# Kernel optimization log

Hardware: AMD Instinct MI355X
Metric: run time of the kernel (lower is better)

The kernel has to match this reference:

```python
import jax, jax.numpy as jnp
import numpy as np

B, N, C, K, D, H = 4, 16000, 128, 16, 4, 512
EPS = 1e-5


def _bn(x, g, b, m, v):
    # eval-mode BatchNorm1d over channel dim (applied to flattened B*N rows)
    return (x - m) * jax.lax.rsqrt(v + EPS) * g + b


def _ffn(x, W1, b1, W2, g, b, m, v):
    h = jax.nn.gelu(jnp.einsum('bnc,ch->bnh', x, W1) + b1)
    y = jnp.einsum('bnh,hc->bnc', h, W2)  # second linear has no bias
    return _bn(y, g, b, m, v)


def _vector_feature(x, knn):
    # knn edge max-pooling: max_k ( x[b, knn[b,n,k], :] - x[b, n, :] )
    gathered = jnp.take_along_axis(x[:, :, None, :], knn[:, :, :, None], axis=1)  # (B,N,K,C)
    return jnp.max(gathered - x[:, :, None, :], axis=2)


def _vfr(x, knn, W, g, b, m, v):
    y = jnp.einsum('bnc,cd->bnd', x, W)
    y = _vector_feature(y, knn)
    return _bn(y, g, b, m, v)


def setup_inputs():
    key = jax.random.key(0)
    ks = jax.random.split(key, 16)
    s = 0.05
    return {
        'x': jax.random.normal(ks[0], (B, N, C), jnp.float32),
        'pe': jax.random.normal(ks[1], (B, N, C), jnp.float32),
        'knn': jax.random.randint(ks[2], (B, N, K), 0, N, dtype=jnp.int32),
        # mlp (the single leading FFN)
        'mlp_W1': jax.random.normal(ks[3], (C, H), jnp.float32) * s,
        'mlp_b1': jnp.zeros((H,), jnp.float32),
        'mlp_W2': jax.random.normal(ks[4], (H, C), jnp.float32) * s,
        'mlp_g': jax.random.uniform(ks[5], (C,), jnp.float32, 0.5, 1.5),
        'mlp_beta': jnp.zeros((C,), jnp.float32),
        'mlp_m': jnp.zeros((C,), jnp.float32),
        'mlp_v': jnp.ones((C,), jnp.float32),
        # per-depth VFR params (stacked over depth D)
        'vfr_W': jax.random.normal(ks[6], (D, C, C), jnp.float32) * s,
        'vfr_g': jax.random.uniform(ks[7], (D, C), jnp.float32, 0.5, 1.5),
        'vfr_beta': jnp.zeros((D, C), jnp.float32),
        'vfr_m': jnp.zeros((D, C), jnp.float32),
        'vfr_v': jnp.ones((D, C), jnp.float32),
        # per-depth FFN params
        'ffn_W1': jax.random.normal(ks[8], (D, C, H), jnp.float32) * s,
        'ffn_b1': jnp.zeros((D, H), jnp.float32),
        'ffn_W2': jax.random.normal(ks[9], (D, H, C), jnp.float32) * s,
        'ffn_g': jax.random.uniform(ks[10], (D, C), jnp.float32, 0.5, 1.5),
        'ffn_beta': jnp.zeros((D, C), jnp.float32),
        'ffn_m': jnp.zeros((D, C), jnp.float32),
        'ffn_v': jnp.ones((D, C), jnp.float32),
    }


def reference(x, pe, knn,
              mlp_W1, mlp_b1, mlp_W2, mlp_g, mlp_beta, mlp_m, mlp_v,
              vfr_W, vfr_g, vfr_beta, vfr_m, vfr_v,
              ffn_W1, ffn_b1, ffn_W2, ffn_g, ffn_beta, ffn_m, ffn_v):
    # drop_path is identity in eval mode
    x = x + _ffn(x, mlp_W1, mlp_b1, mlp_W2, mlp_g, mlp_beta, mlp_m, mlp_v)
    for i in range(D):
        x = x + pe
        x = x + _vfr(x, knn, vfr_W[i], vfr_g[i], vfr_beta[i], vfr_m[i], vfr_v[i])
        x = x + _ffn(x, ffn_W1[i], ffn_b1[i], ffn_W2[i], ffn_g[i], ffn_beta[i], ffn_m[i], ffn_v[i])
    return x
```

## Files before the change

kernel.cpp:

```cpp
#include <hip/hip_runtime.h>
#include <hip/hip_bf16.h>

typedef __attribute__((ext_vector_type(8))) short bf16x8;
typedef __attribute__((ext_vector_type(4))) short bf16x4;
typedef __attribute__((ext_vector_type(4))) float f32x4;

#define B_ 4
#define N_ 16000
#define C_ 128
#define K_ 16
#define D_ 4
#define H_ 512
#define R_ (B_*N_)
#define EPSV 1e-5f

__device__ __forceinline__ ushort f2bf(float f) {
    uint32_t b = __builtin_bit_cast(uint32_t, f);
    b += 0x7fffu + ((b >> 16) & 1u);
    return (ushort)(b >> 16);
}
__device__ __forceinline__ float bf2f(ushort u) {
    return __builtin_bit_cast(float, (uint32_t)u << 16);
}
__device__ __forceinline__ float gelu_fast(float v) {
    float v2 = v * v;
    float u = v * fmaf(0.0356774081f, v2, 0.7978845608f);
    float e = __expf(-2.0f * u);
    return v * __builtin_amdgcn_rcpf(1.0f + e);
}
__device__ __forceinline__ void gll16(const void* g, void* l) {
    __builtin_amdgcn_global_load_lds(
        (__attribute__((address_space(1))) void*)g,
        (__attribute__((address_space(3))) void*)l, 16, 0, 0);
}

__global__ void prep_kernel(
    const float* __restrict__ mlp_W1, const float* __restrict__ mlp_b1,
    const float* __restrict__ mlp_W2, const float* __restrict__ mlp_g,
    const float* __restrict__ mlp_be, const float* __restrict__ mlp_m,
    const float* __restrict__ mlp_v,
    const float* __restrict__ vfr_W, const float* __restrict__ vfr_g,
    const float* __restrict__ vfr_be, const float* __restrict__ vfr_m,
    const float* __restrict__ vfr_v,
    const float* __restrict__ ffn_W1, const float* __restrict__ ffn_b1,
    const float* __restrict__ ffn_W2, const float* __restrict__ ffn_g,
    const float* __restrict__ ffn_be, const float* __restrict__ ffn_m,
    const float* __restrict__ ffn_v,
    ushort* __restrict__ w1t, ushort* __restrict__ w2p, ushort* __restrict__ wvs,
    float* __restrict__ b1a, float* __restrict__ fs, float* __restrict__ fb,
    float* __restrict__ vs, float* __restrict__ vb)
{
    int i = blockIdx.x * 256 + threadIdx.x;
    const int NW = 5 * H_ * C_;
    if (i < NW) {
        int f = i / (H_*C_), e = i % (H_*C_);
        int h = e / C_, c = e % C_;
        const float* src = (f == 0) ? mlp_W1 : ffn_W1 + (size_t)(f-1)*C_*H_;
        w1t[i] = f2bf(src[(size_t)c*H_ + h]);
        return;
    }
    i -= NW;
    if (i < NW) {
        int f = i / (H_*C_), e = i % (H_*C_);
        int c = e / H_, p = e % H_;
        int s = p & 31, lam = s >> 3, j = s & 7;
        int h = (p & ~31) + lam*4 + (j & 3) + ((j >> 2) << 4);
        const float* src = (f == 0) ? mlp_W2 : ffn_W2 + (size_t)(f-1)*H_*C_;
        w2p[i] = f2bf(src[(size_t)h*C_ + c]);
        return;
    }
    i -= NW;
    if (i < D_*C_*C_) {
        int d = i / (C_*C_), e = i % (C_*C_);
        int co = e / C_, p = e % C_;
        int s = p & 31, lam = s >> 3, j = s & 7;
        int k = (p & ~31) + lam*4 + (j & 3) + ((j >> 2) << 4);
        wvs[i] = f2bf(vfr_W[(size_t)d*C_*C_ + (size_t)k*C_ + co]);
        return;
    }
    i -= D_*C_*C_;
    if (i < 5*H_) {
        int f = i / H_, h = i % H_;
        b1a[i] = (f == 0) ? mlp_b1[h] : ffn_b1[(f-1)*H_ + h];
        return;
    }
    i -= 5*H_;
    if (i < 5*C_) {
        int f = i / C_, c = i % C_;
        float g  = (f==0) ? mlp_g[c]  : ffn_g[(f-1)*C_ + c];
        float be = (f==0) ? mlp_be[c] : ffn_be[(f-1)*C_ + c];
        float m  = (f==0) ? mlp_m[c]  : ffn_m[(f-1)*C_ + c];
        float v  = (f==0) ? mlp_v[c]  : ffn_v[(f-1)*C_ + c];
        float s = g * rsqrtf(v + EPSV);
        fs[i] = s; fb[i] = be - m * s;
        return;
    }
    i -= 5*C_;
    if (i < D_*C_) {
        float s = vfr_g[i] * rsqrtf(vfr_v[i] + EPSV);
        vs[i] = s; vb[i] = vfr_be[i] - vfr_m[i] * s;
    }
}

template<bool ADD_PE, bool NEXT_T>
__global__ __launch_bounds__(256, 4) void ffn_kernel(
    const float* __restrict__ xin, float* __restrict__ xout,
    const float* __restrict__ pe,
    const ushort* __restrict__ W1t,
    const ushort* __restrict__ W2p,
    const float* __restrict__ b1,
    const float* __restrict__ bns, const float* __restrict__ bnb,
    const ushort* __restrict__ Wvs,
    ushort* __restrict__ tout)
{
    __shared__ __attribute__((aligned(16))) char lds[32768];
    char* W1s = lds;
    char* W2s = lds + 16384;

    const int tid  = threadIdx.x;
    const int m0   = blockIdx.x * 64;
    const int wv   = tid >> 6;
    const int lane = tid & 63;
    const int lr   = lane & 15;
    const int lh   = lane >> 4;

    bf16x8 xa[4];
    {
        const float* xrow = xin + (size_t)(m0 + wv*16 + lr) * C_ + lh*8;
        #pragma unroll
        for (int kk = 0; kk < 4; ++kk) {
            float4 v0 = *(const float4*)(xrow + kk*32);
            float4 v1 = *(const float4*)(xrow + kk*32 + 4);
            bf16x8 pk;
            pk[0]=(short)f2bf(v0.x); pk[1]=(short)f2bf(v0.y);
            pk[2]=(short)f2bf(v0.z); pk[3]=(short)f2bf(v0.w);
            pk[4]=(short)f2bf(v1.x); pk[5]=(short)f2bf(v1.y);
            pk[6]=(short)f2bf(v1.z); pk[7]=(short)f2bf(v1.w);
            xa[kk] = pk;
        }
    }

    f32x4 acc2[8];
    #pragma unroll
    for (int i = 0; i < 8; ++i) acc2[i] = (f32x4){0.f,0.f,0.f,0.f};

    for (int hc = 0; hc < 8; ++hc) {
        const int h0 = hc * 64;
        __syncthreads();
        #pragma unroll
        for (int i = 0; i < 4; ++i) {
            int row = i*16 + wv*4 + (lane >> 4);
            const char* src = (const char*)(W1t + (size_t)(h0 + row) * C_)
                            + (((lane & 15) * 16) ^ ((row & 7) << 4));
            gll16(src, W1s + i*4096 + wv*1024);
        }
        #pragma unroll
        for (int i = 0; i < 4; ++i) {
            int row = i*32 + wv*8 + (lane >> 3);
            const char* src = (const char*)(W2p + (size_t)row * H_ + h0)
                            + (((lane & 7) * 16) ^ ((row & 7) << 4));
            gll16(src, W2s + i*4096 + wv*1024);
        }
        __syncthreads();

        f32x4 acc1[4];
        #pragma unroll
        for (int i = 0; i < 4; ++i) acc1[i] = (f32x4){0.f,0.f,0.f,0.f};
        #pragma unroll
        for (int kk = 0; kk < 4; ++kk) {
            int kb = kk*64 + lh*16;
            #pragma unroll
            for (int nf = 0; nf < 4; ++nf) {
                int rb = nf*16 + lr;
                bf16x8 w1 = *(bf16x8*)(W1s + rb*256 + (kb ^ ((rb&7)<<4)));
                acc1[nf] = __builtin_amdgcn_mfma_f32_16x16x32_bf16(w1, xa[kk], acc1[nf], 0, 0, 0);
            }
        }
        bf16x4 pa[4];
        #pragma unroll
        for (int nf = 0; nf < 4; ++nf) {
            float4 bias = *(const float4*)(b1 + h0 + nf*16 + lh*4);
            bf16x4 p;
            p[0] = (short)f2bf(gelu_fast(acc1[nf][0] + bias.x));
            p[1] = (short)f2bf(gelu_fast(acc1[nf][1] + bias.y));
            p[2] = (short)f2bf(gelu_fast(acc1[nf][2] + bias.z));
            p[3] = (short)f2bf(gelu_fast(acc1[nf][3] + bias.w));
            pa[nf] = p;
        }
        #pragma unroll
        for (int g = 0; g < 2; ++g) {
            bf16x8 af = __builtin_shufflevector(pa[2*g], pa[2*g+1], 0,1,2,3,4,5,6,7);
            int kb = g*64 + lh*16;
            #pragma unroll
            for (int nf = 0; nf < 8; ++nf) {
                int rb = nf*16 + lr;
                bf16x8 w2 = *(bf16x8*)(W2s + rb*128 + (kb ^ ((rb&7)<<4)));
                acc2[nf] = __builtin_amdgcn_mfma_f32_16x16x32_bf16(w2, af, acc2[nf], 0, 0, 0);
            }
        }
    }

    if (NEXT_T) {
        __syncthreads();
        #pragma unroll
        for (int i = 0; i < 8; ++i) {
            int r = i*16 + wv*4 + (lane >> 4);
            const char* src = (const char*)(Wvs + (size_t)r * C_)
                            + (((lane & 15) * 16) ^ ((r & 7) << 4));
            gll16(src, lds + i*4096 + wv*1024);
        }
    }

    const int row = m0 + wv*16 + lr;
    bf16x4 pa2[8];
    #pragma unroll
    for (int nf = 0; nf < 8; ++nf) {
        int c0 = nf*16 + lh*4;
        float4 sv = *(const float4*)(bns + c0);
        float4 bv = *(const float4*)(bnb + c0);
        float4 xi = *(const float4*)(xin + (size_t)row * C_ + c0);
        if (ADD_PE) {
            float4 pv = *(const float4*)(pe + (size_t)row * C_ + c0);
            xi.x += pv.x; xi.y += pv.y; xi.z += pv.z; xi.w += pv.w;
        }
        float4 xo;
        xo.x = xi.x + acc2[nf][0] * sv.x + bv.x;
        xo.y = xi.y + acc2[nf][1] * sv.y + bv.y;
        xo.z = xi.z + acc2[nf][2] * sv.z + bv.z;
        xo.w = xi.w + acc2[nf][3] * sv.w + bv.w;
        *(float4*)(xout + (size_t)row * C_ + c0) = xo;
        if (NEXT_T) {
            bf16x4 p;
            p[0] = (short)f2bf(xo.x); p[1] = (short)f2bf(xo.y);
            p[2] = (short)f2bf(xo.z); p[3] = (short)f2bf(xo.w);
            pa2[nf] = p;
        }
    }

    if (NEXT_T) {
        __syncthreads();
        f32x4 acc3[8];
        #pragma unroll
        for (int i = 0; i < 8; ++i) acc3[i] = (f32x4){0.f,0.f,0.f,0.f};
        #pragma unroll
        for (int g = 0; g < 4; ++g) {
            bf16x8 af = __builtin_shufflevector(pa2[2*g], pa2[2*g+1], 0,1,2,3,4,5,6,7);
            int kb = g*64 + lh*16;
            #pragma unroll
            for (int nf = 0; nf < 8; ++nf) {
                int rb = nf*16 + lr;
                bf16x8 b = *(bf16x8*)(lds + rb*256 + (kb ^ ((rb&7)<<4)));
                acc3[nf] = __builtin_amdgcn_mfma_f32_16x16x32_bf16(af, b, acc3[nf], 0, 0, 0);
            }
        }
        #pragma unroll
        for (int nf = 0; nf < 8; ++nf) {
            int col = nf*16 + lr;
            #pragma unroll
            for (int j = 0; j < 4; ++j) {
                int trow = m0 + wv*16 + lh*4 + j;
                tout[(size_t)trow * C_ + col] = f2bf(acc3[nf][j]);
            }
        }
    }
}

__global__ __launch_bounds__(256) void vfr_gather_kernel(
    float* __restrict__ x, const ushort* __restrict__ t,
    const int* __restrict__ knn,
    const float* __restrict__ s, const float* __restrict__ bb)
{
    const int wv   = threadIdx.x >> 6;
    const int lane = threadIdx.x & 63;
    const int p = blockIdx.x * 4 + wv;
    const int b = p / N_;
    const int base = b * N_;
    const int* kp = knn + (size_t)p * K_;
    const uint* trow = (const uint*)t;

    uint cen = trow[(size_t)p * 64 + lane];
    float c0 = bf2f((ushort)(cen & 0xffffu));
    float c1 = bf2f((ushort)(cen >> 16));
    float m0v = -INFINITY, m1v = -INFINITY;
    #pragma unroll
    for (int k = 0; k < K_; ++k) {
        int idx = kp[k];
        uint g = trow[(size_t)(base + idx) * 64 + lane];
        m0v = fmaxf(m0v, bf2f((ushort)(g & 0xffffu)));
        m1v = fmaxf(m1v, bf2f((ushort)(g >> 16)));
    }
    m0v -= c0; m1v -= c1;

    int c = lane * 2;
    float2 sv = *(const float2*)(s + c);
    float2 bv = *(const float2*)(bb + c);
    size_t o = (size_t)p * C_ + c;
    float2 xv = *(const float2*)(x + o);
    xv.x += m0v * sv.x + bv.x;
    xv.y += m1v * sv.y + bv.y;
    *(float2*)(x + o) = xv;
}

extern "C" void kernel_launch(void* const* d_in, const int* in_sizes, int n_in,
                              void* d_out, int out_size, void* d_ws, size_t ws_size,
                              hipStream_t stream) {
    const float* x      = (const float*)d_in[0];
    const float* pe     = (const float*)d_in[1];
    const int*   knn    = (const int*)d_in[2];
    const float* mlp_W1 = (const float*)d_in[3];
    const float* mlp_b1 = (const float*)d_in[4];
    const float* mlp_W2 = (const float*)d_in[5];
    const float* mlp_g  = (const float*)d_in[6];
    const float* mlp_be = (const float*)d_in[7];
    const float* mlp_m  = (const float*)d_in[8];
    const float* mlp_v  = (const float*)d_in[9];
    const float* vfr_W  = (const float*)d_in[10];
    const float* vfr_g  = (const float*)d_in[11];
    const float* vfr_be = (const float*)d_in[12];
    const float* vfr_m  = (const float*)d_in[13];
    const float* vfr_v  = (const float*)d_in[14];
    const float* ffn_W1 = (const float*)d_in[15];
    const float* ffn_b1 = (const float*)d_in[16];
    const float* ffn_W2 = (const float*)d_in[17];
    const float* ffn_g  = (const float*)d_in[18];
    const float* ffn_be = (const float*)d_in[19];
    const float* ffn_m  = (const float*)d_in[20];
    const float* ffn_v  = (const float*)d_in[21];
    float* out = (float*)d_out;

    char* ws = (char*)d_ws;
    ushort* tbuf = (ushort*)ws;  ws += (size_t)R_ * C_ * 2;
    ushort* w1t  = (ushort*)ws;  ws += (size_t)5 * H_ * C_ * 2;
    ushort* w2p  = (ushort*)ws;  ws += (size_t)5 * C_ * H_ * 2;
    ushort* wvs  = (ushort*)ws;  ws += (size_t)D_ * C_ * C_ * 2;
    float*  b1a  = (float*)ws;   ws += (size_t)5 * H_ * 4;
    float*  fs   = (float*)ws;   ws += (size_t)5 * C_ * 4;
    float*  fb   = (float*)ws;   ws += (size_t)5 * C_ * 4;
    float*  vs   = (float*)ws;   ws += (size_t)D_ * C_ * 4;
    float*  vb   = (float*)ws;   ws += (size_t)D_ * C_ * 4;

    const int prep_items = 2*(5*H_*C_) + D_*C_*C_ + 5*H_ + 5*C_ + D_*C_;
    prep_kernel<<<(prep_items + 255) / 256, 256, 0, stream>>>(
        mlp_W1, mlp_b1, mlp_W2, mlp_g, mlp_be, mlp_m, mlp_v,
        vfr_W, vfr_g, vfr_be, vfr_m, vfr_v,
        ffn_W1, ffn_b1, ffn_W2, ffn_g, ffn_be, ffn_m, ffn_v,
        w1t, w2p, wvs, b1a, fs, fb, vs, vb);

    ffn_kernel<true, true><<<R_/64, 256, 0, stream>>>(
        x, out, pe, w1t, w2p, b1a, fs, fb, wvs, tbuf);

    for (int d = 0; d < D_; ++d) {
        vfr_gather_kernel<<<R_/4, 256, 0, stream>>>(
            out, tbuf, knn, vs + d * C_, vb + d * C_);
        if (d < D_ - 1) {
            ffn_kernel<true, true><<<R_/64, 256, 0, stream>>>(
                out, out, pe,
                w1t + (size_t)(d+1) * H_ * C_, w2p + (size_t)(d+1) * C_ * H_,
                b1a + (d+1) * H_, fs + (d+1) * C_, fb + (d+1) * C_,
                wvs + (size_t)(d+1) * C_ * C_, tbuf);
        } else {
            ffn_kernel<false, false><<<R_/64, 256, 0, stream>>>(
                out, out, pe,
                w1t + (size_t)(d+1) * H_ * C_, w2p + (size_t)(d+1) * C_ * H_,
                b1a + (d+1) * H_, fs + (d+1) * C_, fb + (d+1) * C_,
                wvs, tbuf);
        }
    }
}
```

Baseline: 350.9 us.

## Double the FFN row tile and double-buffer weight chunks in LDS

Each FFN block now handles 128 rows instead of 64, with each wave computing two 16-row M tiles. Every weight fragment read from LDS therefore feeds two MFMAs, halving weight staging traffic per row. The weight chunks are double-buffered in a 64KB LDS region so the next chunk's global-to-LDS load overlaps the current chunk's compute, leaving one barrier per iteration. In exchange register pressure roughly doubles, launch bounds drop to 2 blocks per CU, and the grid halves to 500 blocks, which may reduce occupancy and latency hiding.

```diff
diff --git a/kernel.cpp b/kernel.cpp
--- a/kernel.cpp
+++ b/kernel.cpp
@@ -21,6 +21,9 @@
 }
 __device__ __forceinline__ float bf2f(ushort u) {
     return __builtin_bit_cast(float, (uint32_t)u << 16);
+}
+__device__ __forceinline__ uint pk2bf(float lo, float hi) {
+    return (uint)f2bf(lo) | ((uint)f2bf(hi) << 16);
 }
 __device__ __forceinline__ float gelu_fast(float v) {
     float v2 = v * v;
@@ -103,7 +106,7 @@
 }
 
 template<bool ADD_PE, bool NEXT_T>
-__global__ __launch_bounds__(256, 4) void ffn_kernel(
+__global__ __launch_bounds__(256, 2) void ffn_kernel(
     const float* __restrict__ xin, float* __restrict__ xout,
     const float* __restrict__ pe,
     const ushort* __restrict__ W1t,
@@ -113,59 +116,72 @@
     const ushort* __restrict__ Wvs,
     ushort* __restrict__ tout)
 {
-    __shared__ __attribute__((aligned(16))) char lds[32768];
-    char* W1s = lds;
-    char* W2s = lds + 16384;
+    __shared__ __attribute__((aligned(16))) char lds[65536];
 
     const int tid  = threadIdx.x;
-    const int m0   = blockIdx.x * 64;
+    const int m0   = blockIdx.x * 128;
     const int wv   = tid >> 6;
     const int lane = tid & 63;
     const int lr   = lane & 15;
     const int lh   = lane >> 4;
 
-    bf16x8 xa[4];
-    {
-        const float* xrow = xin + (size_t)(m0 + wv*16 + lr) * C_ + lh*8;
-        #pragma unroll
-        for (int kk = 0; kk < 4; ++kk) {
-            float4 v0 = *(const float4*)(xrow + kk*32);
-            float4 v1 = *(const float4*)(xrow + kk*32 + 4);
-            bf16x8 pk;
-            pk[0]=(short)f2bf(v0.x); pk[1]=(short)f2bf(v0.y);
-            pk[2]=(short)f2bf(v0.z); pk[3]=(short)f2bf(v0.w);
-            pk[4]=(short)f2bf(v1.x); pk[5]=(short)f2bf(v1.y);
-            pk[6]=(short)f2bf(v1.z); pk[7]=(short)f2bf(v1.w);
-            xa[kk] = pk;
-        }
-    }
-
-    f32x4 acc2[8];
-    #pragma unroll
-    for (int i = 0; i < 8; ++i) acc2[i] = (f32x4){0.f,0.f,0.f,0.f};
-
-    for (int hc = 0; hc < 8; ++hc) {
+    auto stageW = [&](int hc, int buf) {
+        char* base = lds + buf * 32768;
         const int h0 = hc * 64;
-        __syncthreads();
         #pragma unroll
         for (int i = 0; i < 4; ++i) {
             int row = i*16 + wv*4 + (lane >> 4);
             const char* src = (const char*)(W1t + (size_t)(h0 + row) * C_)
                             + (((lane & 15) * 16) ^ ((row & 7) << 4));
-            gll16(src, W1s + i*4096 + wv*1024);
+            gll16(src, base + i*4096 + wv*1024);
         }
         #pragma unroll
         for (int i = 0; i < 4; ++i) {
             int row = i*32 + wv*8 + (lane >> 3);
             const char* src = (const char*)(W2p + (size_t)row * H_ + h0)
                             + (((lane & 7) * 16) ^ ((row & 7) << 4));
-            gll16(src, W2s + i*4096 + wv*1024);
-        }
-        __syncthreads();
-
-        f32x4 acc1[4];
-        #pragma unroll
-        for (int i = 0; i < 4; ++i) acc1[i] = (f32x4){0.f,0.f,0.f,0.f};
+            gll16(src, base + 16384 + i*4096 + wv*1024);
+        }
+    };
+
+    stageW(0, 0);
+
+    bf16x8 xa[2][4];
+    #pragma unroll
+    for (int mt = 0; mt < 2; ++mt) {
+        const float* xrow = xin + (size_t)(m0 + wv*32 + mt*16 + lr) * C_ + lh*8;
+        #pragma unroll
+        for (int kk = 0; kk < 4; ++kk) {
+            float4 v0 = *(const float4*)(xrow + kk*32);
+            float4 v1 = *(const float4*)(xrow + kk*32 + 4);
+            uint p0 = pk2bf(v0.x, v0.y), p1 = pk2bf(v0.z, v0.w);
+            uint p2 = pk2bf(v1.x, v1.y), p3 = pk2bf(v1.z, v1.w);
+            uint4 u = {p0, p1, p2, p3};
+            xa[mt][kk] = __builtin_bit_cast(bf16x8, u);
+        }
+    }
+
+    f32x4 acc2[2][8];
+    #pragma unroll
+    for (int mt = 0; mt < 2; ++mt)
+        #pragma unroll
+        for (int i = 0; i < 8; ++i) acc2[mt][i] = (f32x4){0.f,0.f,0.f,0.f};
+
+    __syncthreads();
+
+    for (int hc = 0; hc < 8; ++hc) {
+        const int h0  = hc * 64;
+        const int buf = hc & 1;
+        if (hc < 7) stageW(hc + 1, buf ^ 1);
+
+        char* W1s = lds + buf * 32768;
+        char* W2s = W1s + 16384;
+
+        f32x4 acc1[2][4];
+        #pragma unroll
+        for (int mt = 0; mt < 2; ++mt)
+            #pragma unroll
+            for (int i = 0; i < 4; ++i) acc1[mt][i] = (f32x4){0.f,0.f,0.f,0.f};
         #pragma unroll
         for (int kk = 0; kk < 4; ++kk) {
             int kb = kk*64 + lh*16;
@@ -173,35 +189,48 @@
             for (int nf = 0; nf < 4; ++nf) {
                 int rb = nf*16 + lr;
                 bf16x8 w1 = *(bf16x8*)(W1s + rb*256 + (kb ^ ((rb&7)<<4)));
-                acc1[nf] = __builtin_amdgcn_mfma_f32_16x16x32_bf16(w1, xa[kk], acc1[nf], 0, 0, 0);
-            }
-        }
-        bf16x4 pa[4];
+                #pragma unroll
+                for (int mt = 0; mt < 2; ++mt)
+                    acc1[mt][nf] = __builtin_amdgcn_mfma_f32_16x16x32_bf16(
+                        w1, xa[mt][kk], acc1[mt][nf], 0, 0, 0);
+            }
+        }
+        bf16x4 pa[2][4];
         #pragma unroll
         for (int nf = 0; nf < 4; ++nf) {
             float4 bias = *(const float4*)(b1 + h0 + nf*16 + lh*4);
-            bf16x4 p;
-            p[0] = (short)f2bf(gelu_fast(acc1[nf][0] + bias.x));
-            p[1] = (short)f2bf(gelu_fast(acc1[nf][1] + bias.y));
-            p[2] = (short)f2bf(gelu_fast(acc1[nf][2] + bias.z));
-            p[3] = (short)f2bf(gelu_fast(acc1[nf][3] + bias.w));
-            pa[nf] = p;
+            #pragma unroll
+            for (int mt = 0; mt < 2; ++mt) {
+                uint q0 = pk2bf(gelu_fast(acc1[mt][nf][0] + bias.x),
+                                gelu_fast(acc1[mt][nf][1] + bias.y));
+                uint q1 = pk2bf(gelu_fast(acc1[mt][nf][2] + bias.z),
+                                gelu_fast(acc1[mt][nf][3] + bias.w));
+                uint2 u = {q0, q1};
+                pa[mt][nf] = __builtin_bit_cast(bf16x4, u);
+            }
         }
         #pragma unroll
         for (int g = 0; g < 2; ++g) {
-            bf16x8 af = __builtin_shufflevector(pa[2*g], pa[2*g+1], 0,1,2,3,4,5,6,7);
+            bf16x8 af[2];
+            #pragma unroll
+            for (int mt = 0; mt < 2; ++mt)
+                af[mt] = __builtin_shufflevector(pa[mt][2*g], pa[mt][2*g+1],
+                                                 0,1,2,3,4,5,6,7);
             int kb = g*64 + lh*16;
             #pragma unroll
             for (int nf = 0; nf < 8; ++nf) {
                 int rb = nf*16 + lr;
                 bf16x8 w2 = *(bf16x8*)(W2s + rb*128 + (kb ^ ((rb&7)<<4)));
-                acc2[nf] = __builtin_amdgcn_mfma_f32_16x16x32_bf16(w2, af, acc2[nf], 0, 0, 0);
-            }
-        }
+                #pragma unroll
+                for (int mt = 0; mt < 2; ++mt)
+                    acc2[mt][nf] = __builtin_amdgcn_mfma_f32_16x16x32_bf16(
+                        w2, af[mt], acc2[mt][nf], 0, 0, 0);
+            }
+        }
+        __syncthreads();
     }
 
     if (NEXT_T) {
-        __syncthreads();
         #pragma unroll
         for (int i = 0; i < 8; ++i) {
             int r = i*16 + wv*4 + (lane >> 4);
@@ -211,55 +240,68 @@
         }
     }
 
-    const int row = m0 + wv*16 + lr;
-    bf16x4 pa2[8];
+    bf16x4 pa2[2][8];
     #pragma unroll
-    for (int nf = 0; nf < 8; ++nf) {
-        int c0 = nf*16 + lh*4;
-        float4 sv = *(const float4*)(bns + c0);
-        float4 bv = *(const float4*)(bnb + c0);
-        float4 xi = *(const float4*)(xin + (size_t)row * C_ + c0);
-        if (ADD_PE) {
-            float4 pv = *(const float4*)(pe + (size_t)row * C_ + c0);
-            xi.x += pv.x; xi.y += pv.y; xi.z += pv.z; xi.w += pv.w;
-        }
-        float4 xo;
-        xo.x = xi.x + acc2[nf][0] * sv.x + bv.x;
-        xo.y = xi.y + acc2[nf][1] * sv.y + bv.y;
-        xo.z = xi.z + acc2[nf][2] * sv.z + bv.z;
-        xo.w = xi.w + acc2[nf][3] * sv.w + bv.w;
-        *(float4*)(xout + (size_t)row * C_ + c0) = xo;
-        if (NEXT_T) {
-            bf16x4 p;
-            p[0] = (short)f2bf(xo.x); p[1] = (short)f2bf(xo.y);
-            p[2] = (short)f2bf(xo.z); p[3] = (short)f2bf(xo.w);
-            pa2[nf] = p;
+    for (int mt = 0; mt < 2; ++mt) {
+        const int row = m0 + wv*32 + mt*16 + lr;
+        #pragma unroll
+        for (int nf = 0; nf < 8; ++nf) {
+            int c0 = nf*16 + lh*4;
+            float4 sv = *(const float4*)(bns + c0);
+            float4 bv = *(const float4*)(bnb + c0);
+            float4 xi = *(const float4*)(xin + (size_t)row * C_ + c0);
+            if (ADD_PE) {
+                float4 pv = *(const float4*)(pe + (size_t)row * C_ + c0);
+                xi.x += pv.x; xi.y += pv.y; xi.z += pv.z; xi.w += pv.w;
+            }
+            float4 xo;
+            xo.x = xi.x + acc2[mt][nf][0] * sv.x + bv.x;
+            xo.y = xi.y + acc2[mt][nf][1] * sv.y + bv.y;
+            xo.z = xi.z + acc2[mt][nf][2] * sv.z + bv.z;
+            xo.w = xi.w + acc2[mt][nf][3] * sv.w + bv.w;
+            *(float4*)(xout + (size_t)row * C_ + c0) = xo;
+            if (NEXT_T) {
+                uint2 u = {pk2bf(xo.x, xo.y), pk2bf(xo.z, xo.w)};
+                pa2[mt][nf] = __builtin_bit_cast(bf16x4, u);
+            }
         }
     }
 
     if (NEXT_T) {
         __syncthreads();
-        f32x4 acc3[8];
-        #pragma unroll
-        for (int i = 0; i < 8; ++i) acc3[i] = (f32x4){0.f,0.f,0.f,0.f};
+        f32x4 acc3[2][8];
+        #pragma unroll
+        for (int mt = 0; mt < 2; ++mt)
+            #pragma unroll
+            for (int i = 0; i < 8; ++i) acc3[mt][i] = (f32x4){0.f,0.f,0.f,0.f};
         #pragma unroll
         for (int g = 0; g < 4; ++g) {
-            bf16x8 af = __builtin_shufflevector(pa2[2*g], pa2[2*g+1], 0,1,2,3,4,5,6,7);
+            bf16x8 af[2];
+            #pragma unroll
+            for (int mt = 0; mt < 2; ++mt)
+                af[mt] = __builtin_shufflevector(pa2[mt][2*g], pa2[mt][2*g+1],
+                                                 0,1,2,3,4,5,6,7);
             int kb = g*64 + lh*16;
             #pragma unroll
             for (int nf = 0; nf < 8; ++nf) {
                 int rb = nf*16 + lr;
-                bf16x8 b = *(bf16x8*)(lds + rb*256 + (kb ^ ((rb&7)<<4)));
-                acc3[nf] = __builtin_amdgcn_mfma_f32_16x16x32_bf16(af, b, acc3[nf], 0, 0, 0);
-            }
-        }
-        #pragma unroll
-        for (int nf = 0; nf < 8; ++nf) {
-            int col = nf*16 + lr;
-            #pragma unroll
-            for (int j = 0; j < 4; ++j) {
-                int trow = m0 + wv*16 + lh*4 + j;
-                tout[(size_t)trow * C_ + col] = f2bf(acc3[nf][j]);
+                bf16x8 wvf = *(bf16x8*)(lds + rb*256 + (kb ^ ((rb&7)<<4)));
+                #pragma unroll
+                for (int mt = 0; mt < 2; ++mt)
+                    acc3[mt][nf] = __builtin_amdgcn_mfma_f32_16x16x32_bf16(
+                        af[mt], wvf, acc3[mt][nf], 0, 0, 0);
+            }
+        }
+        #pragma unroll
+        for (int mt = 0; mt < 2; ++mt) {
+            #pragma unroll
+            for (int nf = 0; nf < 8; ++nf) {
+                int col = nf*16 + lr;
+                #pragma unroll
+                for (int j = 0; j < 4; ++j) {
+                    int trow = m0 + wv*32 + mt*16 + lh*4 + j;
+                    tout[(size_t)trow * C_ + col] = f2bf(acc3[mt][nf][j]);
+                }
             }
         }
     }
@@ -346,20 +388,20 @@
         ffn_W1, ffn_b1, ffn_W2, ffn_g, ffn_be, ffn_m, ffn_v,
         w1t, w2p, wvs, b1a, fs, fb, vs, vb);
 
-    ffn_kernel<true, true><<<R_/64, 256, 0, stream>>>(
+    ffn_kernel<true, true><<<R_/128, 256, 0, stream>>>(
         x, out, pe, w1t, w2p, b1a, fs, fb, wvs, tbuf);
 
     for (int d = 0; d < D_; ++d) {
         vfr_gather_kernel<<<R_/4, 256, 0, stream>>>(
             out, tbuf, knn, vs + d * C_, vb + d * C_);
         if (d < D_ - 1) {
-            ffn_kernel<true, true><<<R_/64, 256, 0, stream>>>(
+            ffn_kernel<true, true><<<R_/128, 256, 0, stream>>>(
                 out, out, pe,
                 w1t + (size_t)(d+1) * H_ * C_, w2p + (size_t)(d+1) * C_ * H_,
                 b1a + (d+1) * H_, fs + (d+1) * C_, fb + (d+1) * C_,
                 wvs + (size_t)(d+1) * C_ * C_, tbuf);
         } else {
-            ffn_kernel<false, false><<<R_/64, 256, 0, stream>>>(
+            ffn_kernel<false, false><<<R_/128, 256, 0, stream>>>(
                 out, out, pe,
                 w1t + (size_t)(d+1) * H_ * C_, w2p + (size_t)(d+1) * C_ * H_,
                 b1a + (d+1) * H_, fs + (d+1) * C_, fb + (d+1) * C_,
```

Measured after the change: 355.4 us. About the same (+1.3%).

## Read FFN weight fragments directly from global memory instead of staging through LDS

Applied to the files above, without the earlier changes.

Removes the LDS staging of W1, W2 and the VFR weight tiles, along with all block-level barriers in the FFN kernel. Each wave now loads its MFMA weight fragments straight from global memory and relies on L1/L2 caching, since the weights are small and shared by all blocks. This drops the shared memory allocation, which may allow more blocks per CU, and removes barrier stalls. The cost is that four waves each fetch the same weights with less coalesced 16-byte loads. bf16 packing is also rewritten to convert pairs of values into 32-bit words.

```diff
diff --git a/kernel.cpp b/kernel.cpp
--- a/kernel.cpp
+++ b/kernel.cpp
@@ -22,16 +22,14 @@
 __device__ __forceinline__ float bf2f(ushort u) {
     return __builtin_bit_cast(float, (uint32_t)u << 16);
 }
+__device__ __forceinline__ uint pk2bf(float lo, float hi) {
+    return (uint)f2bf(lo) | ((uint)f2bf(hi) << 16);
+}
 __device__ __forceinline__ float gelu_fast(float v) {
     float v2 = v * v;
     float u = v * fmaf(0.0356774081f, v2, 0.7978845608f);
     float e = __expf(-2.0f * u);
     return v * __builtin_amdgcn_rcpf(1.0f + e);
-}
-__device__ __forceinline__ void gll16(const void* g, void* l) {
-    __builtin_amdgcn_global_load_lds(
-        (__attribute__((address_space(1))) void*)g,
-        (__attribute__((address_space(3))) void*)l, 16, 0, 0);
 }
 
 __global__ void prep_kernel(
@@ -113,10 +111,6 @@
     const ushort* __restrict__ Wvs,
     ushort* __restrict__ tout)
 {
-    __shared__ __attribute__((aligned(16))) char lds[32768];
-    char* W1s = lds;
-    char* W2s = lds + 16384;
-
     const int tid  = threadIdx.x;
     const int m0   = blockIdx.x * 64;
     const int wv   = tid >> 6;
@@ -131,14 +125,16 @@
         for (int kk = 0; kk < 4; ++kk) {
             float4 v0 = *(const float4*)(xrow + kk*32);
             float4 v1 = *(const float4*)(xrow + kk*32 + 4);
-            bf16x8 pk;
-            pk[0]=(short)f2bf(v0.x); pk[1]=(short)f2bf(v0.y);
-            pk[2]=(short)f2bf(v0.z); pk[3]=(short)f2bf(v0.w);
-            pk[4]=(short)f2bf(v1.x); pk[5]=(short)f2bf(v1.y);
-            pk[6]=(short)f2bf(v1.z); pk[7]=(short)f2bf(v1.w);
-            xa[kk] = pk;
-        }
-    }
+            uint p0 = pk2bf(v0.x, v0.y), p1 = pk2bf(v0.z, v0.w);
+            uint p2 = pk2bf(v1.x, v1.y), p3 = pk2bf(v1.z, v1.w);
+            uint4 u = {p0, p1, p2, p3};
+            xa[kk] = __builtin_bit_cast(bf16x8, u);
+        }
+    }
+
+    const ushort* w1base = W1t + (size_t)lr * C_ + lh*8;
+    const ushort* w2base = W2p + (size_t)lr * H_ + lh*8;
+    const ushort* wvbase = Wvs + (size_t)lr * C_ + lh*8;
 
     f32x4 acc2[8];
     #pragma unroll
@@ -146,68 +142,40 @@
 
     for (int hc = 0; hc < 8; ++hc) {
         const int h0 = hc * 64;
-        __syncthreads();
-        #pragma unroll
-        for (int i = 0; i < 4; ++i) {
-            int row = i*16 + wv*4 + (lane >> 4);
-            const char* src = (const char*)(W1t + (size_t)(h0 + row) * C_)
-                            + (((lane & 15) * 16) ^ ((row & 7) << 4));
-            gll16(src, W1s + i*4096 + wv*1024);
-        }
-        #pragma unroll
-        for (int i = 0; i < 4; ++i) {
-            int row = i*32 + wv*8 + (lane >> 3);
-            const char* src = (const char*)(W2p + (size_t)row * H_ + h0)
-                            + (((lane & 7) * 16) ^ ((row & 7) << 4));
-            gll16(src, W2s + i*4096 + wv*1024);
-        }
-        __syncthreads();
 
         f32x4 acc1[4];
         #pragma unroll
         for (int i = 0; i < 4; ++i) acc1[i] = (f32x4){0.f,0.f,0.f,0.f};
         #pragma unroll
         for (int kk = 0; kk < 4; ++kk) {
-            int kb = kk*64 + lh*16;
             #pragma unroll
             for (int nf = 0; nf < 4; ++nf) {
-                int rb = nf*16 + lr;
-                bf16x8 w1 = *(bf16x8*)(W1s + rb*256 + (kb ^ ((rb&7)<<4)));
-                acc1[nf] = __builtin_amdgcn_mfma_f32_16x16x32_bf16(w1, xa[kk], acc1[nf], 0, 0, 0);
+                bf16x8 w1 = *(const bf16x8*)(w1base + (size_t)(h0 + nf*16) * C_ + kk*32);
+                acc1[nf] = __builtin_amdgcn_mfma_f32_16x16x32_bf16(
+                    w1, xa[kk], acc1[nf], 0, 0, 0);
             }
         }
         bf16x4 pa[4];
         #pragma unroll
         for (int nf = 0; nf < 4; ++nf) {
             float4 bias = *(const float4*)(b1 + h0 + nf*16 + lh*4);
-            bf16x4 p;
-            p[0] = (short)f2bf(gelu_fast(acc1[nf][0] + bias.x));
-            p[1] = (short)f2bf(gelu_fast(acc1[nf][1] + bias.y));
-            p[2] = (short)f2bf(gelu_fast(acc1[nf][2] + bias.z));
-            p[3] = (short)f2bf(gelu_fast(acc1[nf][3] + bias.w));
-            pa[nf] = p;
+            uint q0 = pk2bf(gelu_fast(acc1[nf][0] + bias.x),
+                            gelu_fast(acc1[nf][1] + bias.y));
+            uint q1 = pk2bf(gelu_fast(acc1[nf][2] + bias.z),
+                            gelu_fast(acc1[nf][3] + bias.w));
+            uint2 u = {q0, q1};
+            pa[nf] = __builtin_bit_cast(bf16x4, u);
         }
         #pragma unroll
         for (int g = 0; g < 2; ++g) {
-            bf16x8 af = __builtin_shufflevector(pa[2*g], pa[2*g+1], 0,1,2,3,4,5,6,7);
-            int kb = g*64 + lh*16;
+            bf16x8 af = __builtin_shufflevector(pa[2*g], pa[2*g+1],
+                                                0,1,2,3,4,5,6,7);
             #pragma unroll
             for (int nf = 0; nf < 8; ++nf) {
-                int rb = nf*16 + lr;
-                bf16x8 w2 = *(bf16x8*)(W2s + rb*128 + (kb ^ ((rb&7)<<4)));
-                acc2[nf] = __builtin_amdgcn_mfma_f32_16x16x32_bf16(w2, af, acc2[nf], 0, 0, 0);
+                bf16x8 w2 = *(const bf16x8*)(w2base + (size_t)(nf*16) * H_ + h0 + g*32);
+                acc2[nf] = __builtin_amdgcn_mfma_f32_16x16x32_bf16(
+                    w2, af, acc2[nf], 0, 0, 0);
             }
-        }
-    }
-
-    if (NEXT_T) {
-        __syncthreads();
-        #pragma unroll
-        for (int i = 0; i < 8; ++i) {
-            int r = i*16 + wv*4 + (lane >> 4);
-            const char* src = (const char*)(Wvs + (size_t)r * C_)
-                            + (((lane & 15) * 16) ^ ((r & 7) << 4));
-            gll16(src, lds + i*4096 + wv*1024);
         }
     }
 
@@ -230,27 +198,24 @@
         xo.w = xi.w + acc2[nf][3] * sv.w + bv.w;
         *(float4*)(xout + (size_t)row * C_ + c0) = xo;
         if (NEXT_T) {
-            bf16x4 p;
-            p[0] = (short)f2bf(xo.x); p[1] = (short)f2bf(xo.y);
-            p[2] = (short)f2bf(xo.z); p[3] = (short)f2bf(xo.w);
-            pa2[nf] = p;
+            uint2 u = {pk2bf(xo.x, xo.y), pk2bf(xo.z, xo.w)};
+            pa2[nf] = __builtin_bit_cast(bf16x4, u);
         }
     }
 
     if (NEXT_T) {
-        __syncthreads();
         f32x4 acc3[8];
         #pragma unroll
         for (int i = 0; i < 8; ++i) acc3[i] = (f32x4){0.f,0.f,0.f,0.f};
         #pragma unroll
         for (int g = 0; g < 4; ++g) {
-            bf16x8 af = __builtin_shufflevector(pa2[2*g], pa2[2*g+1], 0,1,2,3,4,5,6,7);
-            int kb = g*64 + lh*16;
+            bf16x8 af = __builtin_shufflevector(pa2[2*g], pa2[2*g+1],
+                                                0,1,2,3,4,5,6,7);
             #pragma unroll
             for (int nf = 0; nf < 8; ++nf) {
-                int rb = nf*16 + lr;
-                bf16x8 b = *(bf16x8*)(lds + rb*256 + (kb ^ ((rb&7)<<4)));
-                acc3[nf] = __builtin_amdgcn_mfma_f32_16x16x32_bf16(af, b, acc3[nf], 0, 0, 0);
+                bf16x8 wvf = *(const bf16x8*)(wvbase + (size_t)(nf*16) * C_ + g*32);
+                acc3[nf] = __builtin_amdgcn_mfma_f32_16x16x32_bf16(
+                    af, wvf, acc3[nf], 0, 0, 0);
             }
         }
         #pragma unroll
```

New measurement: 845.1 us. 141% more time.
